# Performance work log

Hardware: AMD Instinct MI355X
Metric: run time of the kernel (lower is better)

Reference implementation:

```python
import jax, jax.numpy as jnp
import numpy as np

H = 8          # multihead_num (also groups of the Conv1d)
LN_EPS = 1e-5  # torch.nn.LayerNorm default


def _gconv(x, w):
    """Grouped Conv1d, kernel=3, stride=1, 'same' reflect padding, no bias.
    x: [B, C_in, L], w: [C_out, C_in//H, K] (torch OIH layout)."""
    xp = jnp.pad(x, ((0, 0), (0, 0), (1, 1)), mode='reflect')
    return jax.lax.conv_general_dilated(
        xp, w, window_strides=(1,), padding='VALID',
        feature_group_count=H, dimension_numbers=('NCH', 'OIH', 'NCH'))


def setup_inputs() -> dict:
    key = jax.random.key(0)
    ks = jax.random.split(key, 5)
    B, C, L = 8, 512, 1024
    q = jax.random.normal(ks[0], (B, C, L), jnp.float32)
    k = jax.random.normal(ks[1], (B, C, L), jnp.float32)
    # causal mask: 1 above the diagonal -> -1e9 subtracted pre-softmax
    mask = jnp.triu(jnp.ones((L, L), jnp.float32), k=1)
    # init_params: std = sqrt(2 / (C_out + C_in/groups))
    std = float(np.sqrt(2.0 / (C + C // H)))
    wq = jax.random.normal(ks[2], (C, C // H, 3), jnp.float32) * std
    wk = jax.random.normal(ks[3], (C, C // H, 3), jnp.float32) * std
    wv = jax.random.normal(ks[4], (C, C // H, 3), jnp.float32) * std
    gamma = jnp.ones((C,), jnp.float32)
    beta = jnp.zeros((C,), jnp.float32)
    return {"q": q, "k": k, "mask": mask, "wq": wq, "wk": wk, "wv": wv,
            "gamma": gamma, "beta": beta}


def reference(q, k, mask, wq, wk, wv, gamma, beta):
    init = q                               # residual branch, [B, C, L]
    B, C, L = q.shape
    D = C // H                             # head dim
    v = k                                  # inputs list of length 2 -> v = k

    qh = _gconv(q, wq).reshape(B, H, D, L)  # split(dim=1)+cat(dim=0) == head axis
    kh = _gconv(k, wk).reshape(B, H, D, L)
    vh = _gconv(v, wv).reshape(B, H, D, L)

    # scores: q^T k per head; NOTE: scaled by sqrt(multihead_num), as in source
    scores = jnp.einsum('bhdl,bhdm->bhlm', qh, kh) / jnp.sqrt(
        jnp.asarray(H, qh.dtype))
    scores = scores - 1e9 * mask           # mask broadcast over [B, H]
    att = jax.nn.softmax(scores, axis=-1)  # dropout p=0.0 -> identity

    # o = att @ v^T, then concat heads along channel (head-major order)
    o = jnp.einsum('bhlm,bhdm->blhd', att, vh).reshape(B, L, C)

    # residual add + LayerNorm over channel dim
    x = o + jnp.swapaxes(init, 1, 2)       # [B, L, C]
    mu = jnp.mean(x, axis=-1, keepdims=True)
    var = jnp.mean(jnp.square(x - mu), axis=-1, keepdims=True)
    y = (x - mu) * jax.lax.rsqrt(var + LN_EPS) * gamma + beta
    return jnp.swapaxes(y, 1, 2)           # [B, C, L]
```

## Files before the change

kernel.cpp:

```cpp
#include <hip/hip_runtime.h>
#include <math.h>

#define H 8
#define B 8
#define C 512
#define L 1024
#define D 64
#define LDK 72

typedef __attribute__((ext_vector_type(4))) float f32x4;
typedef __attribute__((ext_vector_type(8))) short bf16x8;

static __device__ __forceinline__ short f2bf(float x) {
    union { float f; unsigned u; } v; v.f = x;
    unsigned r = v.u + 0x7FFFu + ((v.u >> 16) & 1u);
    return (short)(r >> 16);
}
static __device__ __forceinline__ short f2bf_fast(float x) {
    union { float f; unsigned u; } v; v.f = x;
    return (short)((v.u + 0x8000u) >> 16);
}
static __device__ __forceinline__ int pack2(short a, short b) {
    return (int)((unsigned short)a | ((unsigned)(unsigned short)b << 16));
}
static __device__ __forceinline__ float bfs2f(short v) {
    union { unsigned u; float f; } w; w.u = ((unsigned)(unsigned short)v) << 16;
    return w.f;
}
static __device__ __forceinline__ void async16(const void* g, void* s) {
    __builtin_amdgcn_global_load_lds(
        (const __attribute__((address_space(1))) int*)g,
        (__attribute__((address_space(3))) int*)s, 16, 0, 0);
}

__global__ __launch_bounds__(256) void wprep_kernel(
    const float* __restrict__ wq, const float* __restrict__ wk,
    const float* __restrict__ wv, short* __restrict__ wtg)
{
    int idx = blockIdx.x * 256 + threadIdx.x;
    int jj    = idx & 7;
    int quad  = (idx >> 3) & 3;
    int d     = (idx >> 5) & 63;
    int r     = idx >> 11;
    int khalf = r & 1;  r >>= 1;
    int t     = r % 3;  r /= 3;
    int h     = r & 7;
    int conv  = r >> 3;
    const float* w = (conv == 0) ? wq : (conv == 1) ? wk : wv;
    int j_in = khalf * 32 + quad * 8 + jj;
    float v = w[(h * 64 + d) * 192 + j_in * 3 + t];
    if (conv == 0) v *= 0.51012254f;
    wtg[idx] = f2bf(v);
}

__global__ __launch_bounds__(256) void conv_kernel(
    const float* __restrict__ q, const float* __restrict__ k,
    const short* __restrict__ wtg,
    short* __restrict__ qh, short* __restrict__ kh, short* __restrict__ vh)
{
    int bx   = blockIdx.x;
    int xcd  = bx & 7;
    int g    = bx >> 3;
    int bh   = xcd + 8 * (g & 7);
    int src  = (g >> 3) & 1;
    int tile = g >> 4;
    int h    = bh & 7;
    int b    = bh >> 3;

    __shared__ __align__(16) short xT[66 * LDK];

    int l0  = tile * 64;
    int tid = threadIdx.x;
    int wave = tid >> 6, lane = tid & 63;
    int n = lane & 15, quad = lane >> 4;

    const float* x  = src ? k : q;
    const float* xb = x + (size_t)(b * C + h * 64) * L + l0;

    int c0 = src ? 1 : 0;
    const short* wb0 = wtg + (size_t)((c0 * 8 + h) * 3 * 2) * 2048;
    bf16x8 wf[3][2], wf2[3][2];
    #pragma unroll
    for (int t = 0; t < 3; t++)
        #pragma unroll
        for (int kk = 0; kk < 2; kk++)
            wf[t][kk] = *(const bf16x8*)(wb0 + (t * 2 + kk) * 2048
                                         + (wave * 16 + n) * 32 + quad * 8);
    if (src) {
        const short* wb1 = wtg + (size_t)((2 * 8 + h) * 3 * 2) * 2048;
        #pragma unroll
        for (int t = 0; t < 3; t++)
            #pragma unroll
            for (int kk = 0; kk < 2; kk++)
                wf2[t][kk] = *(const bf16x8*)(wb1 + (t * 2 + kk) * 2048
                                              + (wave * 16 + n) * 32 + quad * 8);
    }

    {
        #pragma unroll
        for (int s = 0; s < 4; s++) {
            int idx = tid + s * 256;
            int j = idx >> 4, seg = idx & 15;
            float4 v = *(const float4*)(xb + j * L + seg * 4);
            int p = 1 + seg * 4;
            xT[(p + 0) * LDK + j] = f2bf(v.x);
            xT[(p + 1) * LDK + j] = f2bf(v.y);
            xT[(p + 2) * LDK + j] = f2bf(v.z);
            xT[(p + 3) * LDK + j] = f2bf(v.w);
        }
        if (tid < 64) {
            int gl = (l0 == 0) ? 1 : (l0 - 1);
            xT[0 * LDK + tid] = f2bf(x[(size_t)(b * C + h * 64 + tid) * L + gl]);
        } else if (tid < 128) {
            int j2 = tid - 64;
            int gl = (l0 + 64 >= L) ? (L - 2) : (l0 + 64);
            xT[65 * LDK + j2] = f2bf(x[(size_t)(b * C + h * 64 + j2) * L + gl]);
        }
    }
    __syncthreads();

    f32x4 acc[4], acc2[4];
    #pragma unroll
    for (int bl = 0; bl < 4; bl++) {
        acc[bl]  = (f32x4){0.f, 0.f, 0.f, 0.f};
        acc2[bl] = (f32x4){0.f, 0.f, 0.f, 0.f};
    }

    #pragma unroll
    for (int bl = 0; bl < 4; bl++) {
        #pragma unroll
        for (int t = 0; t < 3; t++) {
            #pragma unroll
            for (int kk = 0; kk < 2; kk++) {
                bf16x8 bf = *(const bf16x8*)&xT[(bl * 16 + n + t) * LDK
                                                + kk * 32 + quad * 8];
                acc[bl] = __builtin_amdgcn_mfma_f32_16x16x32_bf16(
                    wf[t][kk], bf, acc[bl], 0, 0, 0);
                if (src)
                    acc2[bl] = __builtin_amdgcn_mfma_f32_16x16x32_bf16(
                        wf2[t][kk], bf, acc2[bl], 0, 0, 0);
            }
        }
    }

    int bhh = bh;
    short* o1 = src ? kh : qh;
    {
        short* ob = o1 + ((size_t)(bhh * 16 + tile)) * 4096;
        int ch = wave * 2 + (quad >> 1);
        #pragma unroll
        for (int bl = 0; bl < 4; bl++) {
            int l = bl * 16 + n;
            int phys = ch ^ (l & 7);
            int2 v;
            v.x = pack2(f2bf(acc[bl][0]), f2bf(acc[bl][1]));
            v.y = pack2(f2bf(acc[bl][2]), f2bf(acc[bl][3]));
            *(int2*)&ob[l * 64 + phys * 8 + (quad & 1) * 4] = v;
        }
    }
    if (src) {
        __syncthreads();
        #pragma unroll
        for (int bl = 0; bl < 4; bl++)
            #pragma unroll
            for (int r = 0; r < 4; r++) {
                int d = wave * 16 + quad * 4 + r;
                int l = bl * 16 + n;
                int phys = (bl * 2 + (n >> 3)) ^ (d & 7);
                xT[d * 64 + phys * 8 + (n & 7)] = f2bf(acc2[bl][r]);
            }
        __syncthreads();
        short* vb = vh + ((size_t)(bhh * 16 + tile)) * 4096;
        #pragma unroll
        for (int jj = 0; jj < 2; jj++) {
            int i = tid + jj * 256;
            *(int4*)(vb + i * 8) = *(const int4*)&xT[i * 8];
        }
    }
}

__global__ __launch_bounds__(256, 4) void flash_kernel(
    const short* __restrict__ qh, const short* __restrict__ kh,
    const short* __restrict__ vh, short* __restrict__ ot)
{
    __shared__ __align__(16) short lds[20480];

    int bx  = blockIdx.x;
    int xcd = bx & 7;
    int g   = bx >> 3;
    int bh  = xcd + 8 * (g & 7);
    int qt  = 15 - (g >> 3);
    int h  = bh & 7, b = bh >> 3;

    int tid  = threadIdx.x;
    int wave = tid >> 6, lane = tid & 63;
    int n    = lane & 15, quad = lane >> 4;

    const short* Qg    = qh + ((size_t)(bh * 16 + qt)) * 4096;
    const short* Kbase = kh + (size_t)bh * 65536;
    const short* Vbase = vh + (size_t)bh * 65536;

    {
        int ci = wave * 64 + lane;
        async16((const int4*)Qg + ci,           lds + wave * 512);
        async16((const int4*)Qg + ci + 256,     lds + 2048 + wave * 512);
        async16((const int4*)Kbase + ci,        lds + 4096 + wave * 512);
        async16((const int4*)Kbase + ci + 256,  lds + 4096 + 2048 + wave * 512);
        async16((const int4*)Vbase + ci,        lds + 8192 + wave * 512);
        async16((const int4*)Vbase + ci + 256,  lds + 8192 + 2048 + wave * 512);
    }
    __syncthreads();

    int ph0 = quad ^ (n & 7);
    int ph1 = (quad + 4) ^ (n & 7);

    bf16x8 qa0 = *(const bf16x8*)&lds[(wave * 16 + n) * 64 + ph0 * 8];
    bf16x8 qa1 = *(const bf16x8*)&lds[(wave * 16 + n) * 64 + ph1 * 8];

    const bf16x8 ones = {16256,16256,16256,16256,16256,16256,16256,16256};

    f32x4 O0 = {0.f,0.f,0.f,0.f}, O1 = O0, O2 = O0, O3 = O0;
    f32x4 Lacc = {0.f,0.f,0.f,0.f};

    int prow   = wave * 16 + n;
    int pswz   = n & 7;

    for (int kt = 0; kt <= qt; kt++) {
        if (kt > 0) __syncthreads();
        if (kt < qt) {
            const short* Kg = Kbase + (size_t)(kt + 1) * 4096;
            const short* Vg = Vbase + (size_t)(kt + 1) * 4096;
            int koff = 4096 + (((kt + 1) & 1)) * 8192;
            int ci = wave * 64 + lane;
            async16((const int4*)Kg + ci,       lds + koff + wave * 512);
            async16((const int4*)Kg + ci + 256, lds + koff + 2048 + wave * 512);
            async16((const int4*)Vg + ci,       lds + koff + 4096 + wave * 512);
            async16((const int4*)Vg + ci + 256, lds + koff + 4096 + 2048 + wave * 512);
        }
        const short* Kb = lds + 4096 + (kt & 1) * 8192;
        const short* Vb = Kb + 4096;

        f32x4 s[4];
        #pragma unroll
        for (int bk = 0; bk < 4; bk++) {
            int row = bk * 16 + n;
            bf16x8 kb0 = *(const bf16x8*)&Kb[row * 64 + ph0 * 8];
            bf16x8 kb1 = *(const bf16x8*)&Kb[row * 64 + ph1 * 8];
            f32x4 acc = {0.f,0.f,0.f,0.f};
            acc = __builtin_amdgcn_mfma_f32_16x16x32_bf16(kb0, qa0, acc, 0, 0, 0);
            acc = __builtin_amdgcn_mfma_f32_16x16x32_bf16(kb1, qa1, acc, 0, 0, 0);
            s[bk] = acc;
        }

        if (kt == qt) {
            #pragma unroll
            for (int bk = 0; bk < 4; bk++)
                #pragma unroll
                for (int r = 0; r < 4; r++)
                    if (bk * 16 + quad * 4 + r > wave * 16 + n)
                        s[bk][r] = -INFINITY;
        }

        #pragma unroll
        for (int bk = 0; bk < 4; bk++) {
            int pch = (bk * 2 + (quad >> 1)) ^ pswz;
            int2 v;
            v.x = pack2(f2bf_fast(__builtin_amdgcn_exp2f(s[bk][0] - 20.f)),
                        f2bf_fast(__builtin_amdgcn_exp2f(s[bk][1] - 20.f)));
            v.y = pack2(f2bf_fast(__builtin_amdgcn_exp2f(s[bk][2] - 20.f)),
                        f2bf_fast(__builtin_amdgcn_exp2f(s[bk][3] - 20.f)));
            *(int2*)&lds[prow * 64 + pch * 8 + (quad & 1) * 4] = v;
        }

        bf16x8 pa0 = *(const bf16x8*)&lds[prow * 64 + ph0 * 8];
        bf16x8 pa1 = *(const bf16x8*)&lds[prow * 64 + ph1 * 8];

        Lacc = __builtin_amdgcn_mfma_f32_16x16x32_bf16(pa0, ones, Lacc, 0, 0, 0);
        Lacc = __builtin_amdgcn_mfma_f32_16x16x32_bf16(pa1, ones, Lacc, 0, 0, 0);

        #pragma unroll
        for (int bk = 0; bk < 4; bk++) {
            int row = bk * 16 + n;
            bf16x8 v0 = *(const bf16x8*)&Vb[row * 64 + ph0 * 8];
            bf16x8 v1 = *(const bf16x8*)&Vb[row * 64 + ph1 * 8];
            f32x4* Op = (bk == 0) ? &O0 : (bk == 1) ? &O1 : (bk == 2) ? &O2 : &O3;
            *Op = __builtin_amdgcn_mfma_f32_16x16x32_bf16(pa0, v0, *Op, 0, 0, 0);
            *Op = __builtin_amdgcn_mfma_f32_16x16x32_bf16(pa1, v1, *Op, 0, 0, 0);
        }
    }

    float inv[4];
    #pragma unroll
    for (int r = 0; r < 4; r++) inv[r] = 1.f / Lacc[r];

    __syncthreads();
    short* Eb = lds + 4096;
    #pragma unroll
    for (int bk = 0; bk < 4; bk++) {
        f32x4* Op = (bk == 0) ? &O0 : (bk == 1) ? &O1 : (bk == 2) ? &O2 : &O3;
        #pragma unroll
        for (int r = 0; r < 4; r++)
            Eb[(bk * 16 + n) * LDK + wave * 16 + quad * 4 + r] =
                f2bf_fast((*Op)[r] * inv[r]);
    }
    __syncthreads();
    #pragma unroll
    for (int jj = 0; jj < 2; jj++) {
        int i = tid + jj * 256;
        int d = i >> 3, seg = i & 7;
        int4 v = *(const int4*)&Eb[d * LDK + seg * 8];
        *(int4*)(ot + ((size_t)(b * C) + h * 64 + d) * L + qt * 64 + seg * 8) = v;
    }
}

__global__ __launch_bounds__(512) void ln_kernel(
    const short* __restrict__ ot, const float* __restrict__ q,
    const float* __restrict__ gamma, const float* __restrict__ beta,
    float* __restrict__ y)
{
    int bx = blockIdx.x;
    int tile = bx & 31;
    int b = bx >> 5;
    int l0 = tile * 32;
    int tid = threadIdx.x;
    int li_ = tid & 31, cs = tid >> 5;

    __shared__ float sp[16][33], ssp[16][33];
    __shared__ float mu_s[32], rs_s[32];

    size_t base = ((size_t)b * C + cs * 32) * L + l0 + li_;
    const short* otp = ot + base;
    const float* qp  = q + base;

    float xr[32];
    float s = 0.f, ss = 0.f;
    #pragma unroll
    for (int cc = 0; cc < 32; cc++) {
        float x = bfs2f(otp[(size_t)cc * L]) + qp[(size_t)cc * L];
        xr[cc] = x;
        s += x; ss += x * x;
    }
    sp[cs][li_] = s; ssp[cs][li_] = ss;
    __syncthreads();
    if (tid < 32) {
        float t1 = 0.f, t2 = 0.f;
        #pragma unroll
        for (int j = 0; j < 16; j++) { t1 += sp[j][tid]; t2 += ssp[j][tid]; }
        float mean = t1 * (1.f / 512.f);
        float var  = t2 * (1.f / 512.f) - mean * mean;
        mu_s[tid] = mean;
        rs_s[tid] = rsqrtf(var + 1e-5f);
    }
    __syncthreads();
    float mu = mu_s[li_], rs = rs_s[li_];
    float* yp = y + base;
    #pragma unroll
    for (int cc = 0; cc < 32; cc++) {
        int c = cs * 32 + cc;
        yp[(size_t)cc * L] = (xr[cc] - mu) * rs * gamma[c] + beta[c];
    }
}

extern "C" void kernel_launch(void* const* d_in, const int* in_sizes, int n_in,
                              void* d_out, int out_size, void* d_ws, size_t ws_size,
                              hipStream_t stream)
{
    const float* q     = (const float*)d_in[0];
    const float* k     = (const float*)d_in[1];
    const float* wq    = (const float*)d_in[3];
    const float* wk    = (const float*)d_in[4];
    const float* wv    = (const float*)d_in[5];
    const float* gamma = (const float*)d_in[6];
    const float* beta  = (const float*)d_in[7];
    float* y = (float*)d_out;

    const size_t N = (size_t)B * H * L * D;
    short* qh  = (short*)d_ws;
    short* kh  = qh + N;
    short* vh  = kh + N;
    short* ot  = vh + N;
    short* wtg = ot + N;

    wprep_kernel<<<1152, 256, 0, stream>>>(wq, wk, wv, wtg);
    conv_kernel<<<2 * B * H * (L / 64), 256, 0, stream>>>(q, k, wtg, qh, kh, vh);
    flash_kernel<<<B * H * (L / 64), 256, 0, stream>>>(qh, kh, vh, ot);
    ln_kernel<<<B * (L / 32), 512, 0, stream>>>(ot, q, gamma, beta, y);
}
```

Before: 134.5 us.

## Fuse conv, flash attention and layernorm into one persistent kernel with counters

Merges the conv, flash-attention and LayerNorm kernels into a single 1024-block kernel. Each block computes its K/V conv tile, publishes it through a per-(b,h) atomic counter, computes its Q projection straight into LDS instead of global memory, then waits on the counter before attention. After attention, half the blocks wait on a per-(b,q-tile) counter and apply LayerNorm to a 16-column slice. This removes two kernel launches, the qh global round trip and the separate LN pass. In exchange it adds spin-wait dependencies that assume all dependent blocks are co-resident (1024 blocks at 4 per CU), and it carries a deadlock risk if they are not.

```diff
diff --git a/kernel.cpp b/kernel.cpp
--- a/kernel.cpp
+++ b/kernel.cpp
@@ -32,11 +32,16 @@
         (const __attribute__((address_space(1))) int*)g,
         (__attribute__((address_space(3))) int*)s, 16, 0, 0);
 }
+static __device__ __forceinline__ unsigned ld_relaxed(const unsigned* p) {
+    return __hip_atomic_load(p, __ATOMIC_RELAXED, __HIP_MEMORY_SCOPE_AGENT);
+}
 
 __global__ __launch_bounds__(256) void wprep_kernel(
     const float* __restrict__ wq, const float* __restrict__ wk,
-    const float* __restrict__ wv, short* __restrict__ wtg)
+    const float* __restrict__ wv, short* __restrict__ wtg,
+    unsigned* __restrict__ cnt)
 {
+    if (blockIdx.x == 0 && threadIdx.x < 192) cnt[threadIdx.x] = 0u;
     int idx = blockIdx.x * 256 + threadIdx.x;
     int jj    = idx & 7;
     int quad  = (idx >> 3) & 3;
@@ -53,50 +58,43 @@
     wtg[idx] = f2bf(v);
 }
 
-__global__ __launch_bounds__(256) void conv_kernel(
+__global__ __launch_bounds__(256, 4) void mega_kernel(
     const float* __restrict__ q, const float* __restrict__ k,
     const short* __restrict__ wtg,
-    short* __restrict__ qh, short* __restrict__ kh, short* __restrict__ vh)
+    short* __restrict__ kh, short* __restrict__ vh, short* __restrict__ ot,
+    unsigned* __restrict__ kcnt, unsigned* __restrict__ ocnt,
+    const float* __restrict__ gamma, const float* __restrict__ beta,
+    float* __restrict__ y)
 {
-    int bx   = blockIdx.x;
-    int xcd  = bx & 7;
-    int g    = bx >> 3;
-    int bh   = xcd + 8 * (g & 7);
-    int src  = (g >> 3) & 1;
-    int tile = g >> 4;
-    int h    = bh & 7;
-    int b    = bh >> 3;
-
-    __shared__ __align__(16) short xT[66 * LDK];
-
-    int l0  = tile * 64;
-    int tid = threadIdx.x;
+    __shared__ __align__(16) short lds[20480];
+    short* xT = &lds[4096];
+
+    int bx  = blockIdx.x;
+    int xcd = bx & 7;
+    int g   = bx >> 3;
+    int bh  = xcd + 8 * (g & 7);
+    int qt  = 15 - (g >> 3);
+    int h   = bh & 7, b = bh >> 3;
+
+    int tid  = threadIdx.x;
     int wave = tid >> 6, lane = tid & 63;
-    int n = lane & 15, quad = lane >> 4;
-
-    const float* x  = src ? k : q;
-    const float* xb = x + (size_t)(b * C + h * 64) * L + l0;
-
-    int c0 = src ? 1 : 0;
-    const short* wb0 = wtg + (size_t)((c0 * 8 + h) * 3 * 2) * 2048;
-    bf16x8 wf[3][2], wf2[3][2];
-    #pragma unroll
-    for (int t = 0; t < 3; t++)
-        #pragma unroll
-        for (int kk = 0; kk < 2; kk++)
-            wf[t][kk] = *(const bf16x8*)(wb0 + (t * 2 + kk) * 2048
-                                         + (wave * 16 + n) * 32 + quad * 8);
-    if (src) {
-        const short* wb1 = wtg + (size_t)((2 * 8 + h) * 3 * 2) * 2048;
+    int n    = lane & 15, quad = lane >> 4;
+    int l0   = qt * 64;
+
+    {
+        const float* xb = k + (size_t)(b * C + h * 64) * L + l0;
+        const short* wb0 = wtg + (size_t)((1 * 8 + h) * 6) * 2048;
+        const short* wb1 = wtg + (size_t)((2 * 8 + h) * 6) * 2048;
+        bf16x8 wf[3][2], wf2[3][2];
         #pragma unroll
         for (int t = 0; t < 3; t++)
             #pragma unroll
-            for (int kk = 0; kk < 2; kk++)
+            for (int kk = 0; kk < 2; kk++) {
+                wf[t][kk]  = *(const bf16x8*)(wb0 + (t * 2 + kk) * 2048
+                                              + (wave * 16 + n) * 32 + quad * 8);
                 wf2[t][kk] = *(const bf16x8*)(wb1 + (t * 2 + kk) * 2048
                                               + (wave * 16 + n) * 32 + quad * 8);
-    }
-
-    {
+            }
         #pragma unroll
         for (int s = 0; s < 4; s++) {
             int idx = tid + s * 256;
@@ -110,43 +108,113 @@
         }
         if (tid < 64) {
             int gl = (l0 == 0) ? 1 : (l0 - 1);
-            xT[0 * LDK + tid] = f2bf(x[(size_t)(b * C + h * 64 + tid) * L + gl]);
+            xT[0 * LDK + tid] = f2bf(k[(size_t)(b * C + h * 64 + tid) * L + gl]);
         } else if (tid < 128) {
             int j2 = tid - 64;
             int gl = (l0 + 64 >= L) ? (L - 2) : (l0 + 64);
-            xT[65 * LDK + j2] = f2bf(x[(size_t)(b * C + h * 64 + j2) * L + gl]);
-        }
-    }
-    __syncthreads();
-
-    f32x4 acc[4], acc2[4];
-    #pragma unroll
-    for (int bl = 0; bl < 4; bl++) {
-        acc[bl]  = (f32x4){0.f, 0.f, 0.f, 0.f};
-        acc2[bl] = (f32x4){0.f, 0.f, 0.f, 0.f};
-    }
-
-    #pragma unroll
-    for (int bl = 0; bl < 4; bl++) {
-        #pragma unroll
-        for (int t = 0; t < 3; t++) {
-            #pragma unroll
-            for (int kk = 0; kk < 2; kk++) {
-                bf16x8 bf = *(const bf16x8*)&xT[(bl * 16 + n + t) * LDK
-                                                + kk * 32 + quad * 8];
-                acc[bl] = __builtin_amdgcn_mfma_f32_16x16x32_bf16(
-                    wf[t][kk], bf, acc[bl], 0, 0, 0);
-                if (src)
+            xT[65 * LDK + j2] = f2bf(k[(size_t)(b * C + h * 64 + j2) * L + gl]);
+        }
+        __syncthreads();
+
+        f32x4 acc[4], acc2[4];
+        #pragma unroll
+        for (int bl = 0; bl < 4; bl++) {
+            acc[bl]  = (f32x4){0.f, 0.f, 0.f, 0.f};
+            acc2[bl] = (f32x4){0.f, 0.f, 0.f, 0.f};
+        }
+        #pragma unroll
+        for (int bl = 0; bl < 4; bl++)
+            #pragma unroll
+            for (int t = 0; t < 3; t++)
+                #pragma unroll
+                for (int kk = 0; kk < 2; kk++) {
+                    bf16x8 bf = *(const bf16x8*)&xT[(bl * 16 + n + t) * LDK
+                                                    + kk * 32 + quad * 8];
+                    acc[bl]  = __builtin_amdgcn_mfma_f32_16x16x32_bf16(
+                        wf[t][kk],  bf, acc[bl],  0, 0, 0);
                     acc2[bl] = __builtin_amdgcn_mfma_f32_16x16x32_bf16(
                         wf2[t][kk], bf, acc2[bl], 0, 0, 0);
+                }
+
+        {
+            short* ob = kh + ((size_t)(bh * 16 + qt)) * 4096;
+            int ch = wave * 2 + (quad >> 1);
+            #pragma unroll
+            for (int bl = 0; bl < 4; bl++) {
+                int l = bl * 16 + n;
+                int phys = ch ^ (l & 7);
+                int2 v;
+                v.x = pack2(f2bf(acc[bl][0]), f2bf(acc[bl][1]));
+                v.y = pack2(f2bf(acc[bl][2]), f2bf(acc[bl][3]));
+                *(int2*)&ob[l * 64 + phys * 8 + (quad & 1) * 4] = v;
             }
         }
-    }
-
-    int bhh = bh;
-    short* o1 = src ? kh : qh;
+        __syncthreads();
+        #pragma unroll
+        for (int bl = 0; bl < 4; bl++)
+            #pragma unroll
+            for (int r = 0; r < 4; r++) {
+                int d = wave * 16 + quad * 4 + r;
+                int l = bl * 16 + n;
+                int phys = (bl * 2 + (n >> 3)) ^ (d & 7);
+                xT[d * 64 + phys * 8 + (n & 7)] = f2bf(acc2[bl][r]);
+            }
+        __syncthreads();
+        short* vb = vh + ((size_t)(bh * 16 + qt)) * 4096;
+        #pragma unroll
+        for (int jj = 0; jj < 2; jj++) {
+            int i = tid + jj * 256;
+            *(int4*)(vb + i * 8) = *(const int4*)&xT[i * 8];
+        }
+        __syncthreads();
+        if (tid == 0) { __threadfence(); atomicAdd(&kcnt[bh], 1u); }
+    }
+
     {
-        short* ob = o1 + ((size_t)(bhh * 16 + tile)) * 4096;
+        const float* xb = q + (size_t)(b * C + h * 64) * L + l0;
+        const short* wb0 = wtg + (size_t)((0 * 8 + h) * 6) * 2048;
+        bf16x8 wf[3][2];
+        #pragma unroll
+        for (int t = 0; t < 3; t++)
+            #pragma unroll
+            for (int kk = 0; kk < 2; kk++)
+                wf[t][kk] = *(const bf16x8*)(wb0 + (t * 2 + kk) * 2048
+                                             + (wave * 16 + n) * 32 + quad * 8);
+        #pragma unroll
+        for (int s = 0; s < 4; s++) {
+            int idx = tid + s * 256;
+            int j = idx >> 4, seg = idx & 15;
+            float4 v = *(const float4*)(xb + j * L + seg * 4);
+            int p = 1 + seg * 4;
+            xT[(p + 0) * LDK + j] = f2bf(v.x);
+            xT[(p + 1) * LDK + j] = f2bf(v.y);
+            xT[(p + 2) * LDK + j] = f2bf(v.z);
+            xT[(p + 3) * LDK + j] = f2bf(v.w);
+        }
+        if (tid < 64) {
+            int gl = (l0 == 0) ? 1 : (l0 - 1);
+            xT[0 * LDK + tid] = f2bf(q[(size_t)(b * C + h * 64 + tid) * L + gl]);
+        } else if (tid < 128) {
+            int j2 = tid - 64;
+            int gl = (l0 + 64 >= L) ? (L - 2) : (l0 + 64);
+            xT[65 * LDK + j2] = f2bf(q[(size_t)(b * C + h * 64 + j2) * L + gl]);
+        }
+        __syncthreads();
+
+        f32x4 acc[4];
+        #pragma unroll
+        for (int bl = 0; bl < 4; bl++) acc[bl] = (f32x4){0.f, 0.f, 0.f, 0.f};
+        #pragma unroll
+        for (int bl = 0; bl < 4; bl++)
+            #pragma unroll
+            for (int t = 0; t < 3; t++)
+                #pragma unroll
+                for (int kk = 0; kk < 2; kk++) {
+                    bf16x8 bf = *(const bf16x8*)&xT[(bl * 16 + n + t) * LDK
+                                                    + kk * 32 + quad * 8];
+                    acc[bl] = __builtin_amdgcn_mfma_f32_16x16x32_bf16(
+                        wf[t][kk], bf, acc[bl], 0, 0, 0);
+                }
         int ch = wave * 2 + (quad >> 1);
         #pragma unroll
         for (int bl = 0; bl < 4; bl++) {
@@ -155,55 +223,20 @@
             int2 v;
             v.x = pack2(f2bf(acc[bl][0]), f2bf(acc[bl][1]));
             v.y = pack2(f2bf(acc[bl][2]), f2bf(acc[bl][3]));
-            *(int2*)&ob[l * 64 + phys * 8 + (quad & 1) * 4] = v;
-        }
-    }
-    if (src) {
-        __syncthreads();
-        #pragma unroll
-        for (int bl = 0; bl < 4; bl++)
-            #pragma unroll
-            for (int r = 0; r < 4; r++) {
-                int d = wave * 16 + quad * 4 + r;
-                int l = bl * 16 + n;
-                int phys = (bl * 2 + (n >> 3)) ^ (d & 7);
-                xT[d * 64 + phys * 8 + (n & 7)] = f2bf(acc2[bl][r]);
-            }
-        __syncthreads();
-        short* vb = vh + ((size_t)(bhh * 16 + tile)) * 4096;
-        #pragma unroll
-        for (int jj = 0; jj < 2; jj++) {
-            int i = tid + jj * 256;
-            *(int4*)(vb + i * 8) = *(const int4*)&xT[i * 8];
-        }
-    }
-}
-
-__global__ __launch_bounds__(256, 4) void flash_kernel(
-    const short* __restrict__ qh, const short* __restrict__ kh,
-    const short* __restrict__ vh, short* __restrict__ ot)
-{
-    __shared__ __align__(16) short lds[20480];
-
-    int bx  = blockIdx.x;
-    int xcd = bx & 7;
-    int g   = bx >> 3;
-    int bh  = xcd + 8 * (g & 7);
-    int qt  = 15 - (g >> 3);
-    int h  = bh & 7, b = bh >> 3;
-
-    int tid  = threadIdx.x;
-    int wave = tid >> 6, lane = tid & 63;
-    int n    = lane & 15, quad = lane >> 4;
-
-    const short* Qg    = qh + ((size_t)(bh * 16 + qt)) * 4096;
+            *(int2*)&lds[l * 64 + phys * 8 + (quad & 1) * 4] = v;
+        }
+    }
+
     const short* Kbase = kh + (size_t)bh * 65536;
     const short* Vbase = vh + (size_t)bh * 65536;
 
+    if (tid == 0) {
+        while (ld_relaxed(&kcnt[bh]) < 16u) __builtin_amdgcn_s_sleep(2);
+        __threadfence();
+    }
+    __syncthreads();
     {
         int ci = wave * 64 + lane;
-        async16((const int4*)Qg + ci,           lds + wave * 512);
-        async16((const int4*)Qg + ci + 256,     lds + 2048 + wave * 512);
         async16((const int4*)Kbase + ci,        lds + 4096 + wave * 512);
         async16((const int4*)Kbase + ci + 256,  lds + 4096 + 2048 + wave * 512);
         async16((const int4*)Vbase + ci,        lds + 8192 + wave * 512);
@@ -222,8 +255,8 @@
     f32x4 O0 = {0.f,0.f,0.f,0.f}, O1 = O0, O2 = O0, O3 = O0;
     f32x4 Lacc = {0.f,0.f,0.f,0.f};
 
-    int prow   = wave * 16 + n;
-    int pswz   = n & 7;
+    int prow = wave * 16 + n;
+    int pswz = n & 7;
 
     for (int kt = 0; kt <= qt; kt++) {
         if (kt > 0) __syncthreads();
@@ -311,53 +344,54 @@
         int4 v = *(const int4*)&Eb[d * LDK + seg * 8];
         *(int4*)(ot + ((size_t)(b * C) + h * 64 + d) * L + qt * 64 + seg * 8) = v;
     }
-}
-
-__global__ __launch_bounds__(512) void ln_kernel(
-    const short* __restrict__ ot, const float* __restrict__ q,
-    const float* __restrict__ gamma, const float* __restrict__ beta,
-    float* __restrict__ y)
-{
-    int bx = blockIdx.x;
-    int tile = bx & 31;
-    int b = bx >> 5;
-    int l0 = tile * 32;
-    int tid = threadIdx.x;
-    int li_ = tid & 31, cs = tid >> 5;
-
-    __shared__ float sp[16][33], ssp[16][33];
-    __shared__ float mu_s[32], rs_s[32];
-
-    size_t base = ((size_t)b * C + cs * 32) * L + l0 + li_;
-    const short* otp = ot + base;
-    const float* qp  = q + base;
-
-    float xr[32];
-    float s = 0.f, ss = 0.f;
-    #pragma unroll
-    for (int cc = 0; cc < 32; cc++) {
-        float x = bfs2f(otp[(size_t)cc * L]) + qp[(size_t)cc * L];
-        xr[cc] = x;
-        s += x; ss += x * x;
-    }
-    sp[cs][li_] = s; ssp[cs][li_] = ss;
     __syncthreads();
-    if (tid < 32) {
-        float t1 = 0.f, t2 = 0.f;
-        #pragma unroll
-        for (int j = 0; j < 16; j++) { t1 += sp[j][tid]; t2 += ssp[j][tid]; }
-        float mean = t1 * (1.f / 512.f);
-        float var  = t2 * (1.f / 512.f) - mean * mean;
-        mu_s[tid] = mean;
-        rs_s[tid] = rsqrtf(var + 1e-5f);
-    }
-    __syncthreads();
-    float mu = mu_s[li_], rs = rs_s[li_];
-    float* yp = y + base;
-    #pragma unroll
-    for (int cc = 0; cc < 32; cc++) {
-        int c = cs * 32 + cc;
-        yp[(size_t)cc * L] = (xr[cc] - mu) * rs * gamma[c] + beta[c];
+    if (tid == 0) { __threadfence(); atomicAdd(&ocnt[b * 16 + qt], 1u); }
+
+    if (h < 4) {
+        if (tid == 0) {
+            while (ld_relaxed(&ocnt[b * 16 + qt]) < 8u) __builtin_amdgcn_s_sleep(2);
+            __threadfence();
+        }
+        __syncthreads();
+
+        int li_ = tid & 15, cs = tid >> 4;
+        int ll0 = qt * 64 + h * 16;
+        float* sp  = (float*)lds;
+        float* ssp = sp + 272;
+        float* mus = ssp + 272;
+        float* rss = mus + 16;
+
+        size_t base = ((size_t)(b * C + cs * 32)) * L + ll0 + li_;
+        const short* otp = ot + base;
+        const float* qp  = q + base;
+
+        float xr[32];
+        float s = 0.f, ss = 0.f;
+        #pragma unroll
+        for (int cc = 0; cc < 32; cc++) {
+            float x = bfs2f(otp[(size_t)cc * L]) + qp[(size_t)cc * L];
+            xr[cc] = x;
+            s += x; ss += x * x;
+        }
+        sp[cs * 17 + li_] = s; ssp[cs * 17 + li_] = ss;
+        __syncthreads();
+        if (tid < 16) {
+            float t1 = 0.f, t2 = 0.f;
+            #pragma unroll
+            for (int j = 0; j < 16; j++) { t1 += sp[j * 17 + tid]; t2 += ssp[j * 17 + tid]; }
+            float mean = t1 * (1.f / 512.f);
+            float var  = t2 * (1.f / 512.f) - mean * mean;
+            mus[tid] = mean;
+            rss[tid] = rsqrtf(var + 1e-5f);
+        }
+        __syncthreads();
+        float mu = mus[li_], rs = rss[li_];
+        float* yp = y + base;
+        #pragma unroll
+        for (int cc = 0; cc < 32; cc++) {
+            int c = cs * 32 + cc;
+            yp[(size_t)cc * L] = (xr[cc] - mu) * rs * gamma[c] + beta[c];
+        }
     }
 }
 
@@ -375,14 +409,15 @@
     float* y = (float*)d_out;
 
     const size_t N = (size_t)B * H * L * D;
-    short* qh  = (short*)d_ws;
-    short* kh  = qh + N;
+    short* kh  = (short*)d_ws;
     short* vh  = kh + N;
     short* ot  = vh + N;
     short* wtg = ot + N;
-
-    wprep_kernel<<<1152, 256, 0, stream>>>(wq, wk, wv, wtg);
-    conv_kernel<<<2 * B * H * (L / 64), 256, 0, stream>>>(q, k, wtg, qh, kh, vh);
-    flash_kernel<<<B * H * (L / 64), 256, 0, stream>>>(qh, kh, vh, ot);
-    ln_kernel<<<B * (L / 32), 512, 0, stream>>>(ot, q, gamma, beta, y);
-}
+    unsigned* cnt  = (unsigned*)(wtg + 294912);
+    unsigned* kcnt = cnt;
+    unsigned* ocnt = cnt + 64;
+
+    wprep_kernel<<<1152, 256, 0, stream>>>(wq, wk, wv, wtg, cnt);
+    mega_kernel<<<1024, 256, 0, stream>>>(q, k, wtg, kh, vh, ot,
+                                          kcnt, ocnt, gamma, beta, y);
+}
```

Measured after the change: 286.3 us. 2.13x slower.
